# Performance work log

Hardware: AMD Instinct MI355X
Metric: run time of the kernel (lower is better)

The kernel has to match this reference:

```python
import jax, jax.numpy as jnp
import numpy as np

D_MODEL = 512
NUM_HEADS = 8
D_K = D_MODEL // NUM_HEADS


def setup_inputs() -> dict:
    key = jax.random.key(0)
    k0, k1, k2, k3, k4 = jax.random.split(key, 5)
    s = 1.0 / np.sqrt(D_MODEL)
    return {
        "x": jax.random.normal(k0, (2, 4096, D_MODEL), dtype=jnp.float32),
        "W_q": jax.random.normal(k1, (D_MODEL, D_MODEL), dtype=jnp.float32) * s,
        "W_k": jax.random.normal(k2, (D_MODEL, D_MODEL), dtype=jnp.float32) * s,
        "W_v": jax.random.normal(k3, (D_MODEL, D_MODEL), dtype=jnp.float32) * s,
        "W_o": jax.random.normal(k4, (D_MODEL, D_MODEL), dtype=jnp.float32) * s,
    }


def reference(x, W_q, W_k, W_v, W_o):
    B, S, _ = x.shape
    # project and split heads: (B, H, S, d_k)
    def split(t):
        return t.reshape(B, S, NUM_HEADS, D_K).transpose(0, 2, 1, 3)
    Q = split(x @ W_q)
    K = split(x @ W_k)
    V = split(x @ W_v)
    scale = jnp.sqrt(jnp.asarray(D_K, dtype=x.dtype))
    logits = jnp.einsum('bhqd,bhkd->bhqk', Q, K) / scale
    attn = jax.nn.softmax(logits, axis=-1)  # dropout is identity at inference
    out = jnp.einsum('bhqk,bhkd->bhqd', attn, V)
    concat = out.transpose(0, 2, 1, 3).reshape(B, S, D_MODEL)
    return concat @ W_o
```

## Files before the change

kernel.cpp:

```cpp
#include <hip/hip_runtime.h>
#include <hip/hip_bf16.h>


#define DMODEL 512
#define SEQ    4096
#define NTOK   8192
#define LDQK   1024

using f32x4 = __attribute__((ext_vector_type(4))) float;
using s16x8 = __attribute__((ext_vector_type(8))) short;
using u16x8 = __attribute__((ext_vector_type(8))) unsigned short;

static __device__ __forceinline__ unsigned short f2bf(float f) {
  union { float f; unsigned u; } v; v.f = f;
  unsigned r = v.u + 0x7fff + ((v.u >> 16) & 1);
  return (unsigned short)(r >> 16);
}

static __device__ __forceinline__ unsigned pack_bf2(float lo, float hi) {
  __hip_bfloat162 t = __float22bfloat162_rn(make_float2(lo, hi));
  union { __hip_bfloat162 b; unsigned u; } c; c.b = t; return c.u;
}

static __device__ __forceinline__ void gll16(const void* g, void* l) {
  __builtin_amdgcn_global_load_lds(
      (const __attribute__((address_space(1))) unsigned int*)g,
      (__attribute__((address_space(3))) unsigned int*)l, 16, 0, 0);
}

__global__ void prep_kernel(const float* __restrict__ x,
                            const float* __restrict__ Wq,
                            const float* __restrict__ Wk,
                            const float* __restrict__ Wv,
                            const float* __restrict__ Wo,
                            unsigned short* __restrict__ xb,
                            unsigned short* __restrict__ Wall, float c2) {
  __shared__ float T[64][65];
  const int bx = blockIdx.x;
  if (bx < 1024) {
    for (int i = bx * 256 + threadIdx.x; i < NTOK * DMODEL / 4; i += 262144) {
      float4 v = ((const float4*)x)[i];
      ushort4 o;
      o.x = f2bf(v.x); o.y = f2bf(v.y); o.z = f2bf(v.z); o.w = f2bf(v.w);
      ((ushort4*)xb)[i] = o;
    }
    return;
  }
  const int t = bx - 1024;
  const int y = t >> 6, sub = t & 63;
  const float* W = (y == 0) ? Wq : (y == 1) ? Wk : (y == 2) ? Wv : Wo;
  const float scale = (y == 0) ? c2 : 1.0f;
  const int tk = (sub & 7) * 64;
  const int tn = (sub >> 3) * 64;
  const int r  = threadIdx.x >> 2;
  const int cq = threadIdx.x & 3;
#pragma unroll
  for (int i = 0; i < 4; ++i) {
    int c = (cq + 4 * i) * 4;
    float4 v = *(const float4*)&W[(size_t)(tk + r) * 512 + tn + c];
    T[r][c + 0] = v.x * scale; T[r][c + 1] = v.y * scale;
    T[r][c + 2] = v.z * scale; T[r][c + 3] = v.w * scale;
  }
  __syncthreads();
  const int n  = threadIdx.x >> 2;
  const int k0 = (threadIdx.x & 3) * 16;
#pragma unroll
  for (int j4 = 0; j4 < 4; ++j4) {
    ushort4 o;
    o.x = f2bf(T[k0 + j4 * 4 + 0][n]);
    o.y = f2bf(T[k0 + j4 * 4 + 1][n]);
    o.z = f2bf(T[k0 + j4 * 4 + 2][n]);
    o.w = f2bf(T[k0 + j4 * 4 + 3][n]);
    *(ushort4*)&Wall[(size_t)y * 262144 + (size_t)(tn + n) * 512 + tk + k0 + j4 * 4] = o;
  }
}

__global__ __launch_bounds__(256, 3) void gemm_qkv(
    const unsigned short* __restrict__ xb,
    const unsigned short* __restrict__ Wall,
    unsigned short* __restrict__ QKb,
    unsigned short* __restrict__ Vtb)
{
  __shared__ unsigned short As[128 * 32];
  __shared__ unsigned short Bs[128 * 32];
  const int by = blockIdx.y;
  const bool vmode = (by >= 8);
  const unsigned short* A  = vmode ? (Wall + 2 * 262144) : xb;
  const unsigned short* Bt = vmode ? xb : Wall;
  const size_t bm = vmode ? (size_t)(by - 8) * 128 : (size_t)blockIdx.x * 128;
  const size_t bn = vmode ? (size_t)blockIdx.x * 128 : (size_t)by * 128;
  const int tid  = threadIdx.x;
  const int wave = tid >> 6, lane = tid & 63;
  const int q4 = lane >> 4, ln = lane & 15;
  const int wm = (wave >> 1) * 64, wn = (wave & 1) * 64;
  f32x4 acc[4][4] = {};
  const int srow = wave * 16 + (lane >> 2);
  const int scol = (lane & 3) * 8;

  const unsigned short* Ag  = A  + (bm + srow)      * 512 + scol;
  const unsigned short* Ag2 = A  + (bm + 64 + srow) * 512 + scol;
  const unsigned short* Bg  = Bt + (bn + srow)      * 512 + scol;
  const unsigned short* Bg2 = Bt + (bn + 64 + srow) * 512 + scol;
  unsigned short* Ad  = As + wave * 512;
  unsigned short* Ad2 = As + 2048 + wave * 512;
  unsigned short* Bd  = Bs + wave * 512;
  unsigned short* Bd2 = Bs + 2048 + wave * 512;

  for (int kt = 0; kt < 512; kt += 32) {
    __syncthreads();
    gll16(Ag + kt,  Ad);
    gll16(Ag2 + kt, Ad2);
    gll16(Bg + kt,  Bd);
    gll16(Bg2 + kt, Bd2);
    __syncthreads();
    s16x8 af[4], bfr[4];
#pragma unroll
    for (int i = 0; i < 4; i++)
      af[i] = *(const s16x8*)(As + (wm + i * 16 + ln) * 32 + q4 * 8);
#pragma unroll
    for (int i = 0; i < 4; i++)
      bfr[i] = *(const s16x8*)(Bs + (wn + i * 16 + ln) * 32 + q4 * 8);
#pragma unroll
    for (int mi = 0; mi < 4; mi++)
#pragma unroll
      for (int ni = 0; ni < 4; ni++)
        acc[mi][ni] = __builtin_amdgcn_mfma_f32_16x16x32_bf16(
            af[mi], bfr[ni], acc[mi][ni], 0, 0, 0);
  }
#pragma unroll
  for (int mi = 0; mi < 4; mi++)
#pragma unroll
    for (int r = 0; r < 4; ++r) {
      size_t row = bm + wm + mi * 16 + q4 * 4 + r;
#pragma unroll
      for (int ni = 0; ni < 4; ni++) {
        size_t col = bn + wn + ni * 16 + ln;
        unsigned short hv = f2bf(acc[mi][ni][r]);
        if (!vmode) {
          QKb[row * 1024 + col] = hv;
        } else {
          int b = (int)(col >> 12), s = (int)(col & 4095);
          int sp = (s & ~63) | (s & 32) | (((s >> 2) & 3) << 3) |
                   (((s >> 4) & 1) << 2) | (s & 3);
          Vtb[(size_t)b * 2097152 + row * 4096 + sp] = hv;
        }
      }
    }
}

__global__ __launch_bounds__(256, 2) void attn_kernel(
    const unsigned short* __restrict__ QK,
    const unsigned short* __restrict__ Vt,
    float* __restrict__ Opart,
    float* __restrict__ Lpart)
{
  const int qt = blockIdx.x, h = blockIdx.y, z = blockIdx.z;
  const int b = z >> 1, ck = z & 1;
  const int tid = threadIdx.x, wave = tid >> 6, lane = tid & 63;
  const int q4 = lane >> 4, ln = lane & 15;
  __shared__ unsigned short Ks[2][64 * 72];
  __shared__ unsigned short Vs[2][64 * 72];
  const size_t rowbase = (size_t)b * SEQ;
  const size_t qrow0   = (size_t)qt * 128 + wave * 32;
  const unsigned short* Kp  = QK + rowbase * LDQK + 512 + h * 64;
  const unsigned short* VTp = Vt + ((size_t)(b * 8 + h) * 64) * SEQ;

  s16x8 qf[2][2];
#pragma unroll
  for (int mf = 0; mf < 2; ++mf) {
    const unsigned short* q = QK + (rowbase + qrow0 + mf * 16 + ln) * LDQK + h * 64;
    qf[mf][0] = *(const s16x8*)(q + q4 * 8);
    qf[mf][1] = *(const s16x8*)(q + 32 + q4 * 8);
  }
  f32x4 o[2][4] = {};
  float lp[2] = {};

  const int srow = tid >> 2;
  const int scol = (tid & 3) * 16;

  const unsigned short* kgp = Kp  + (size_t)(ck * 2048 + srow) * LDQK + scol;
  const unsigned short* vgp = VTp + (size_t)srow * SEQ + ck * 2048 + scol;

  u16x8 kr  = *(const u16x8*)kgp;
  u16x8 kr2 = *(const u16x8*)(kgp + 8);
  u16x8 vr  = *(const u16x8*)vgp;
  u16x8 vr2 = *(const u16x8*)(vgp + 8);
  *(u16x8*)(Ks[0] + srow * 72 + scol)     = kr;
  *(u16x8*)(Ks[0] + srow * 72 + scol + 8) = kr2;
  *(u16x8*)(Vs[0] + srow * 72 + scol)     = vr;
  *(u16x8*)(Vs[0] + srow * 72 + scol + 8) = vr2;
  kgp += (size_t)64 * LDQK;  vgp += 64;
  kr  = *(const u16x8*)kgp;
  kr2 = *(const u16x8*)(kgp + 8);
  vr  = *(const u16x8*)vgp;
  vr2 = *(const u16x8*)(vgp + 8);
  __syncthreads();

  for (int t = 0; t < 32; ++t) {
    const int cur = t & 1;
    const unsigned short* Kc = Ks[cur];
    const unsigned short* Vc = Vs[cur];

    f32x4 s4[2][4] = {};
#pragma unroll
    for (int ni = 0; ni < 4; ni++) {
      const unsigned short* kb = Kc + (ni * 16 + ln) * 72 + q4 * 8;
      s16x8 kf0 = *(const s16x8*)kb;
      s16x8 kf1 = *(const s16x8*)(kb + 32);
#pragma unroll
      for (int mf = 0; mf < 2; ++mf) {
        s4[mf][ni] = __builtin_amdgcn_mfma_f32_16x16x32_bf16(kf0, qf[mf][0], s4[mf][ni], 0, 0, 0);
        s4[mf][ni] = __builtin_amdgcn_mfma_f32_16x16x32_bf16(kf1, qf[mf][1], s4[mf][ni], 0, 0, 0);
      }
    }
    s16x8 vf[2][4];
#pragma unroll
    for (int ks = 0; ks < 2; ++ks)
#pragma unroll
      for (int ni = 0; ni < 4; ni++)
        vf[ks][ni] = *(const s16x8*)(Vc + (ni * 16 + ln) * 72 + ks * 32 + q4 * 8);

    s16x8 pf[2][2];
#pragma unroll
    for (int mf = 0; mf < 2; ++mf) {
      float e[4][4];
      float ls = 0.f;
#pragma unroll
      for (int ni = 0; ni < 4; ni++)
#pragma unroll
        for (int r = 0; r < 4; ++r) {
          e[ni][r] = __builtin_amdgcn_exp2f(s4[mf][ni][r]);
          ls += e[ni][r];
        }
      lp[mf] += ls;
#pragma unroll
      for (int ks = 0; ks < 2; ++ks) {
        union { s16x8 v; unsigned u[4]; } pu;
        pu.u[0] = pack_bf2(e[2 * ks][0],     e[2 * ks][1]);
        pu.u[1] = pack_bf2(e[2 * ks][2],     e[2 * ks][3]);
        pu.u[2] = pack_bf2(e[2 * ks + 1][0], e[2 * ks + 1][1]);
        pu.u[3] = pack_bf2(e[2 * ks + 1][2], e[2 * ks + 1][3]);
        pf[mf][ks] = pu.v;
      }
    }
#pragma unroll
    for (int ks = 0; ks < 2; ++ks)
#pragma unroll
      for (int ni = 0; ni < 4; ni++)
#pragma unroll
        for (int mf = 0; mf < 2; ++mf)
          o[mf][ni] = __builtin_amdgcn_mfma_f32_16x16x32_bf16(pf[mf][ks], vf[ks][ni], o[mf][ni], 0, 0, 0);

    if (t + 1 < 32) {
      unsigned short* Kn = Ks[cur ^ 1];
      unsigned short* Vn = Vs[cur ^ 1];
      *(u16x8*)(Kn + srow * 72 + scol)     = kr;
      *(u16x8*)(Kn + srow * 72 + scol + 8) = kr2;
      *(u16x8*)(Vn + srow * 72 + scol)     = vr;
      *(u16x8*)(Vn + srow * 72 + scol + 8) = vr2;
      if (t + 2 < 32) {
        kgp += (size_t)64 * LDQK;  vgp += 64;
        kr  = *(const u16x8*)kgp;
        kr2 = *(const u16x8*)(kgp + 8);
        vr  = *(const u16x8*)vgp;
        vr2 = *(const u16x8*)(vgp + 8);
      }
    }
    __syncthreads();
  }
#pragma unroll
  for (int mf = 0; mf < 2; ++mf) {
    float l = lp[mf];
    l += __shfl_xor(l, 16, 64);
    l += __shfl_xor(l, 32, 64);
    if (q4 == 0)
      Lpart[(size_t)ck * 65536 + (size_t)(b * 8 + h) * 4096 + qrow0 + mf * 16 + ln] = l;
  }
  float* Opc = Opart + (size_t)ck * NTOK * DMODEL;
#pragma unroll
  for (int mf = 0; mf < 2; ++mf)
#pragma unroll
    for (int r = 0; r < 4; ++r) {
      size_t row = rowbase + qrow0 + mf * 16 + q4 * 4 + r;
#pragma unroll
      for (int ni = 0; ni < 4; ni++)
        Opc[row * DMODEL + h * 64 + ni * 16 + ln] = o[mf][ni][r];
    }
}

__global__ void combine_kernel(const float* __restrict__ Opart,
                               const float* __restrict__ Lpart,
                               unsigned short* __restrict__ Oc) {
  int i = blockIdx.x * 256 + threadIdx.x;
  int row = i >> 7;
  int c4  = (i & 127) * 4;
  int b = row >> 12, qrow = row & 4095, h = c4 >> 6;
  float l = Lpart[(size_t)(b * 8 + h) * 4096 + qrow] +
            Lpart[65536 + (size_t)(b * 8 + h) * 4096 + qrow];
  float inv = 1.0f / l;
  f32x4 a = *(const f32x4*)(Opart + (size_t)row * 512 + c4);
  f32x4 c = *(const f32x4*)(Opart + (size_t)NTOK * DMODEL + (size_t)row * 512 + c4);
  float r0 = (a[0] + c[0]) * inv, r1 = (a[1] + c[1]) * inv;
  float r2 = (a[2] + c[2]) * inv, r3 = (a[3] + c[3]) * inv;
  uint2 w;
  w.x = pack_bf2(r0, r1);
  w.y = pack_bf2(r2, r3);
  *(uint2*)&Oc[(size_t)row * 512 + c4] = w;
}

__global__ __launch_bounds__(256, 3) void gemm_out(
    const unsigned short* __restrict__ A,
    const unsigned short* __restrict__ Bt,
    float* __restrict__ C)
{
  __shared__ unsigned short As[128 * 32];
  __shared__ unsigned short Bs[64 * 32];
  const int tid  = threadIdx.x;
  const int wave = tid >> 6, lane = tid & 63;
  const int q4 = lane >> 4, ln = lane & 15;
  const size_t bm = (size_t)blockIdx.x * 128;
  const size_t bn = (size_t)blockIdx.y * 64;
  const int wm = (wave >> 1) * 64, wn = (wave & 1) * 32;
  f32x4 acc[4][2] = {};
  const int srow = wave * 16 + (lane >> 2);
  const int scol = (lane & 3) * 8;

  const unsigned short* Ag  = A  + (bm + srow)      * 512 + scol;
  const unsigned short* Ag2 = A  + (bm + 64 + srow) * 512 + scol;
  const unsigned short* Bg  = Bt + (bn + srow)      * 512 + scol;
  unsigned short* Ad  = As + wave * 512;
  unsigned short* Ad2 = As + 2048 + wave * 512;
  unsigned short* Bd  = Bs + wave * 512;

  for (int kt = 0; kt < 512; kt += 32) {
    __syncthreads();
    gll16(Ag + kt,  Ad);
    gll16(Ag2 + kt, Ad2);
    gll16(Bg + kt,  Bd);
    __syncthreads();
    s16x8 af[4], bfr[2];
#pragma unroll
    for (int i = 0; i < 4; i++)
      af[i] = *(const s16x8*)(As + (wm + i * 16 + ln) * 32 + q4 * 8);
#pragma unroll
    for (int i = 0; i < 2; i++)
      bfr[i] = *(const s16x8*)(Bs + (wn + i * 16 + ln) * 32 + q4 * 8);
#pragma unroll
    for (int mi = 0; mi < 4; mi++)
#pragma unroll
      for (int ni = 0; ni < 2; ni++)
        acc[mi][ni] = __builtin_amdgcn_mfma_f32_16x16x32_bf16(
            af[mi], bfr[ni], acc[mi][ni], 0, 0, 0);
  }
#pragma unroll
  for (int mi = 0; mi < 4; mi++)
#pragma unroll
    for (int r = 0; r < 4; ++r) {
      size_t row = bm + wm + mi * 16 + q4 * 4 + r;
#pragma unroll
      for (int ni = 0; ni < 2; ni++)
        C[row * 512 + bn + wn + ni * 16 + ln] = acc[mi][ni][r];
    }
}

extern "C" void kernel_launch(void* const* d_in, const int* in_sizes, int n_in,
                              void* d_out, int out_size, void* d_ws, size_t ws_size,
                              hipStream_t stream) {
  const float* x  = (const float*)d_in[0];
  const float* Wq = (const float*)d_in[1];
  const float* Wk = (const float*)d_in[2];
  const float* Wv = (const float*)d_in[3];
  const float* Wo = (const float*)d_in[4];

  char* ws = (char*)d_ws;
  unsigned short* xb    = (unsigned short*)(ws);
  unsigned short* Wall  = (unsigned short*)(ws + 8388608);
  unsigned short* QKb   = (unsigned short*)(ws + 10485760);
  unsigned short* Vtb   = (unsigned short*)(ws + 27262976);
  unsigned short* Oc    = (unsigned short*)(ws + 35651584);
  float*          Opart = (float*)(ws + 44040192);
  float*          Lpart = (float*)(ws + 77594624);

  const float C2 = 0.125f * 1.44269504088896f;

  hipLaunchKernelGGL(prep_kernel, dim3(1280), dim3(256), 0, stream,
                     x, Wq, Wk, Wv, Wo, xb, Wall, C2);
  hipLaunchKernelGGL(gemm_qkv, dim3(64, 12), dim3(256), 0, stream,
                     xb, Wall, QKb, Vtb);
  hipLaunchKernelGGL(attn_kernel, dim3(32, 8, 4), dim3(256), 0, stream,
                     QKb, Vtb, Opart, Lpart);
  hipLaunchKernelGGL(combine_kernel, dim3(4096), dim3(256), 0, stream,
                     Opart, Lpart, Oc);
  hipLaunchKernelGGL(gemm_out, dim3(64, 8), dim3(256), 0, stream,
                     Oc, Wall + 3 * 262144, (float*)d_out);
}
```

Before: 199.7 us.

## Swizzle K/V shared tiles with XOR layout and raise MFMA wave priority

Replaces the padded 72-element LDS rows for K and V tiles with unpadded 64-element rows using an XOR swizzle on 16-byte chunks, so fragment reads stay conflict-free while LDS use shrinks. It also wraps the MFMA blocks in s_setprio to favour matrix issue, starts the score accumulation from a zero constant instead of zero-initialised registers, and turns the row-sum into a tree. The aim is to cut LDS footprint and bank conflicts and to raise MFMA throughput; the risk is added address arithmetic and priority changes that could unbalance the schedule across waves.

```diff
diff --git a/kernel.cpp b/kernel.cpp
--- a/kernel.cpp
+++ b/kernel.cpp
@@ -158,8 +158,8 @@
   const int b = z >> 1, ck = z & 1;
   const int tid = threadIdx.x, wave = tid >> 6, lane = tid & 63;
   const int q4 = lane >> 4, ln = lane & 15;
-  __shared__ unsigned short Ks[2][64 * 72];
-  __shared__ unsigned short Vs[2][64 * 72];
+  __shared__ unsigned short Ks[2][64 * 64];
+  __shared__ unsigned short Vs[2][64 * 64];
   const size_t rowbase = (size_t)b * SEQ;
   const size_t qrow0   = (size_t)qt * 128 + wave * 32;
   const unsigned short* Kp  = QK + rowbase * LDQK + 512 + h * 64;
@@ -176,19 +176,23 @@
   float lp[2] = {};
 
   const int srow = tid >> 2;
-  const int scol = (tid & 3) * 16;
-
-  const unsigned short* kgp = Kp  + (size_t)(ck * 2048 + srow) * LDQK + scol;
-  const unsigned short* vgp = VTp + (size_t)srow * SEQ + ck * 2048 + scol;
+  const int c32  = (tid & 3) * 32;
+  const int swz  = (srow & 7) << 4;
+  const int wof0 = srow * 128 + ((c32 +  0) ^ swz);
+  const int wof1 = srow * 128 + ((c32 + 16) ^ swz);
+  const int rswz = (ln & 7) << 4;
+
+  const unsigned short* kgp = Kp  + (size_t)(ck * 2048 + srow) * LDQK + (c32 >> 1);
+  const unsigned short* vgp = VTp + (size_t)srow * SEQ + ck * 2048 + (c32 >> 1);
 
   u16x8 kr  = *(const u16x8*)kgp;
   u16x8 kr2 = *(const u16x8*)(kgp + 8);
   u16x8 vr  = *(const u16x8*)vgp;
   u16x8 vr2 = *(const u16x8*)(vgp + 8);
-  *(u16x8*)(Ks[0] + srow * 72 + scol)     = kr;
-  *(u16x8*)(Ks[0] + srow * 72 + scol + 8) = kr2;
-  *(u16x8*)(Vs[0] + srow * 72 + scol)     = vr;
-  *(u16x8*)(Vs[0] + srow * 72 + scol + 8) = vr2;
+  *(u16x8*)((char*)Ks[0] + wof0) = kr;
+  *(u16x8*)((char*)Ks[0] + wof1) = kr2;
+  *(u16x8*)((char*)Vs[0] + wof0) = vr;
+  *(u16x8*)((char*)Vs[0] + wof1) = vr2;
   kgp += (size_t)64 * LDQK;  vgp += 64;
   kr  = *(const u16x8*)kgp;
   kr2 = *(const u16x8*)(kgp + 8);
@@ -196,43 +200,49 @@
   vr2 = *(const u16x8*)(vgp + 8);
   __syncthreads();
 
+  const f32x4 fz = {0.f, 0.f, 0.f, 0.f};
+
   for (int t = 0; t < 32; ++t) {
     const int cur = t & 1;
-    const unsigned short* Kc = Ks[cur];
-    const unsigned short* Vc = Vs[cur];
-
-    f32x4 s4[2][4] = {};
+    const char* Kc = (const char*)Ks[cur];
+    const char* Vc = (const char*)Vs[cur];
+
+    f32x4 s4[2][4];
 #pragma unroll
     for (int ni = 0; ni < 4; ni++) {
-      const unsigned short* kb = Kc + (ni * 16 + ln) * 72 + q4 * 8;
-      s16x8 kf0 = *(const s16x8*)kb;
-      s16x8 kf1 = *(const s16x8*)(kb + 32);
+      const char* kb = Kc + (ni * 16 + ln) * 128;
+      s16x8 kf0 = *(const s16x8*)(kb + ((q4 * 16)      ^ rswz));
+      s16x8 kf1 = *(const s16x8*)(kb + ((q4 * 16 + 64) ^ rswz));
+      __builtin_amdgcn_s_setprio(1);
 #pragma unroll
       for (int mf = 0; mf < 2; ++mf) {
-        s4[mf][ni] = __builtin_amdgcn_mfma_f32_16x16x32_bf16(kf0, qf[mf][0], s4[mf][ni], 0, 0, 0);
-        s4[mf][ni] = __builtin_amdgcn_mfma_f32_16x16x32_bf16(kf1, qf[mf][1], s4[mf][ni], 0, 0, 0);
+        f32x4 acc0 = __builtin_amdgcn_mfma_f32_16x16x32_bf16(kf0, qf[mf][0], fz, 0, 0, 0);
+        s4[mf][ni] = __builtin_amdgcn_mfma_f32_16x16x32_bf16(kf1, qf[mf][1], acc0, 0, 0, 0);
       }
+      __builtin_amdgcn_s_setprio(0);
     }
     s16x8 vf[2][4];
 #pragma unroll
     for (int ks = 0; ks < 2; ++ks)
 #pragma unroll
       for (int ni = 0; ni < 4; ni++)
-        vf[ks][ni] = *(const s16x8*)(Vc + (ni * 16 + ln) * 72 + ks * 32 + q4 * 8);
+        vf[ks][ni] = *(const s16x8*)(Vc + (ni * 16 + ln) * 128 +
+                                     ((ks * 64 + q4 * 16) ^ rswz));
 
     s16x8 pf[2][2];
 #pragma unroll
     for (int mf = 0; mf < 2; ++mf) {
       float e[4][4];
-      float ls = 0.f;
 #pragma unroll
       for (int ni = 0; ni < 4; ni++)
 #pragma unroll
-        for (int r = 0; r < 4; ++r) {
+        for (int r = 0; r < 4; ++r)
           e[ni][r] = __builtin_amdgcn_exp2f(s4[mf][ni][r]);
-          ls += e[ni][r];
-        }
-      lp[mf] += ls;
+      float t0 = (e[0][0] + e[0][1]) + (e[0][2] + e[0][3]);
+      float t1 = (e[1][0] + e[1][1]) + (e[1][2] + e[1][3]);
+      float t2 = (e[2][0] + e[2][1]) + (e[2][2] + e[2][3]);
+      float t3 = (e[3][0] + e[3][1]) + (e[3][2] + e[3][3]);
+      lp[mf] += (t0 + t1) + (t2 + t3);
 #pragma unroll
       for (int ks = 0; ks < 2; ++ks) {
         union { s16x8 v; unsigned u[4]; } pu;
@@ -243,6 +253,7 @@
         pf[mf][ks] = pu.v;
       }
     }
+    __builtin_amdgcn_s_setprio(1);
 #pragma unroll
     for (int ks = 0; ks < 2; ++ks)
 #pragma unroll
@@ -250,14 +261,15 @@
 #pragma unroll
         for (int mf = 0; mf < 2; ++mf)
           o[mf][ni] = __builtin_amdgcn_mfma_f32_16x16x32_bf16(pf[mf][ks], vf[ks][ni], o[mf][ni], 0, 0, 0);
+    __builtin_amdgcn_s_setprio(0);
 
     if (t + 1 < 32) {
-      unsigned short* Kn = Ks[cur ^ 1];
-      unsigned short* Vn = Vs[cur ^ 1];
-      *(u16x8*)(Kn + srow * 72 + scol)     = kr;
-      *(u16x8*)(Kn + srow * 72 + scol + 8) = kr2;
-      *(u16x8*)(Vn + srow * 72 + scol)     = vr;
-      *(u16x8*)(Vn + srow * 72 + scol + 8) = vr2;
+      char* Kn = (char*)Ks[cur ^ 1];
+      char* Vn = (char*)Vs[cur ^ 1];
+      *(u16x8*)(Kn + wof0) = kr;
+      *(u16x8*)(Kn + wof1) = kr2;
+      *(u16x8*)(Vn + wof0) = vr;
+      *(u16x8*)(Vn + wof1) = vr2;
       if (t + 2 < 32) {
         kgp += (size_t)64 * LDQK;  vgp += 64;
         kr  = *(const u16x8*)kgp;
```

Result: faster. 193.2 us (-3.2%).
